# Kernel optimization log

Hardware: AMD Instinct MI355X
Metric: run time of the kernel (lower is better)

The kernel has to match this reference:

```python
import jax, jax.numpy as jnp
import numpy as np

HID = 128   # hidden_dim
NCLS = 10   # n_classes
B = 64      # number of graphs in the batched heterograph
NC, NP, NN = 100000, 400000, 150000  # component / port / net node counts
E = 400000  # edges per edge type


def setup_inputs() -> dict:
    key = jax.random.key(0)
    ks = jax.random.split(key, 32)
    f32 = jnp.float32

    def w(k, shape, fan_in):
        return jax.random.normal(k, shape, dtype=f32) * (1.0 / np.sqrt(fan_in))

    inp = {
        "h_comp": jax.random.normal(ks[0], (NC, 1), f32),
        "h_port": jax.random.normal(ks[1], (NP, 2), f32),
        "h_net": jax.random.normal(ks[2], (NN, 1), f32),
        "e_cp_src": jax.random.randint(ks[3], (E,), 0, NC, dtype=jnp.int32),
        "e_cp_dst": jax.random.randint(ks[4], (E,), 0, NP, dtype=jnp.int32),
        "e_pn_src": jax.random.randint(ks[5], (E,), 0, NP, dtype=jnp.int32),
        "e_pn_dst": jax.random.randint(ks[6], (E,), 0, NN, dtype=jnp.int32),
        "gid_comp": jnp.sort(jax.random.randint(ks[7], (NC,), 0, B, dtype=jnp.int32)),
        "gid_port": jnp.sort(jax.random.randint(ks[8], (NP,), 0, B, dtype=jnp.int32)),
        "gid_net": jnp.sort(jax.random.randint(ks[9], (NN,), 0, B, dtype=jnp.int32)),
        # GraphConv weights/biases per (layer, edge_type)
        "W1_cp": w(ks[10], (1, HID), 1), "b1_cp": jnp.zeros((HID,), f32),
        "W1_pn": w(ks[11], (2, HID), 2), "b1_pn": jnp.zeros((HID,), f32),
        "W2_cp": w(ks[12], (HID, HID), HID), "b2_cp": jnp.zeros((HID,), f32),
        "W2_pn": w(ks[13], (HID, HID), HID), "b2_pn": jnp.zeros((HID,), f32),
        "W3_cp": w(ks[14], (HID, HID), HID), "b3_cp": jnp.zeros((HID,), f32),
        "W3_pn": w(ks[15], (HID, HID), HID), "b3_pn": jnp.zeros((HID,), f32),
        # classify MLP (input dim 4 = 1+2+1 pooled original features)
        "Wc1": w(ks[16], (4, HID), 4), "bc1": jnp.zeros((HID,), f32),
        "Wc2": w(ks[17], (HID, HID), HID), "bc2": jnp.zeros((HID,), f32),
        "Wc3": w(ks[18], (HID, NCLS), HID), "bc3": jnp.zeros((NCLS,), f32),
    }
    return inp


def reference(h_comp, h_port, h_net,
              e_cp_src, e_cp_dst, e_pn_src, e_pn_dst,
              gid_comp, gid_port, gid_net,
              W1_cp, b1_cp, W1_pn, b1_pn,
              W2_cp, b2_cp, W2_pn, b2_pn,
              W3_cp, b3_cp, W3_pn, b3_pn,
              Wc1, bc1, Wc2, bc2, Wc3, bc3):
    seg = jax.ops.segment_sum

    # --- HeteroGraphConv layers (faithful to original forward, including its
    # bug: DGL HeteroGraphConv drops node types with no incoming relation, so
    # 'component' vanishes after conv1 and 'port' after conv2; conv3 runs on an
    # empty dict; conv outputs are never written back to g, hence dead code).
    # GraphConv(norm='none'): dst = sum_{edges} (x_src @ W) + b
    port1 = jax.nn.relu(seg((h_comp @ W1_cp)[e_cp_src], e_cp_dst, num_segments=NP) + b1_cp)
    net1 = jax.nn.relu(seg((h_port @ W1_pn)[e_pn_src], e_pn_dst, num_segments=NN) + b1_pn)
    net2 = jax.nn.relu(seg((port1 @ W2_pn)[e_pn_src], e_pn_dst, num_segments=NN) + b2_pn)
    # conv3: skipped entirely (no src types remain in the feature dict)
    del net1, net2  # never used by the original module's output path

    # --- dgl.mean_nodes reads g.nodes[*].data['h'] = ORIGINAL input features
    def gmean(x, gid):
        s = seg(x, gid, num_segments=B)
        c = seg(jnp.ones((x.shape[0], 1), x.dtype), gid, num_segments=B)
        return s / jnp.maximum(c, 1.0)

    hg = jnp.concatenate([gmean(h_comp, gid_comp),
                          gmean(h_port, gid_port),
                          gmean(h_net, gid_net)], axis=1)  # [B, 4]

    h = jax.nn.relu(hg @ Wc1 + bc1)
    h = jax.nn.relu(h @ Wc2 + bc2)
    return h @ Wc3 + bc3  # [B, n_classes]
```

## Files before the change

kernel.cpp:

```cpp
#include <hip/hip_runtime.h>
#include <hip/hip_bf16.h>


#define NGRAPH 64
#define NB_COMP 40
#define NB_PORT 172
#define NB_NET  44
#define GRID (NB_COMP + NB_PORT + NB_NET)


__device__ __forceinline__ float ws_read(float* p) {
    return atomicAdd(p, 0.0f);
}

template <int NF>
__device__ void reduce_type(const float* __restrict__ h, const int* __restrict__ gid, int n,
                            float* __restrict__ gsum, float* __restrict__ gcnt,
                            float (*bins)[NGRAPH][4],
                            int nblocks, int bid) {
    int nv = (n + 3) >> 2;
    int per = (nv + nblocks - 1) / nblocks;
    int start = bid * per;
    int end = min(nv, start + per);
    int set = threadIdx.x & 3;

    int cur = -1;
    float s0 = 0.f, s1 = 0.f, cnt = 0.f;

    for (int iv = start + (int)threadIdx.x; iv < end; iv += (int)blockDim.x) {
        int i = iv * 4;
        int g[4];
        float v0[4], v1[4];
        if (i + 3 < n) {
            int4 g4 = ((const int4*)gid)[iv];
            g[0] = g4.x; g[1] = g4.y; g[2] = g4.z; g[3] = g4.w;
            if (NF == 1) {
                float4 hv = ((const float4*)h)[iv];
                v0[0] = hv.x; v0[1] = hv.y; v0[2] = hv.z; v0[3] = hv.w;
            } else {
                float4 ha = ((const float4*)h)[iv * 2];
                float4 hb = ((const float4*)h)[iv * 2 + 1];
                v0[0] = ha.x; v1[0] = ha.y; v0[1] = ha.z; v1[1] = ha.w;
                v0[2] = hb.x; v1[2] = hb.y; v0[3] = hb.z; v1[3] = hb.w;
            }
        } else {
#pragma unroll
            for (int t = 0; t < 4; ++t) {
                if (i + t < n) {
                    g[t] = gid[i + t];
                    if (NF == 1) { v0[t] = h[i + t]; }
                    else { v0[t] = h[(i + t) * 2]; v1[t] = h[(i + t) * 2 + 1]; }
                } else {
                    g[t] = -2;
                    v0[t] = 0.f; v1[t] = 0.f;
                }
            }
        }
#pragma unroll
        for (int t = 0; t < 4; ++t) {
            if (g[t] == -2) continue;
            if (g[t] != cur) {
                if (cur >= 0) {
                    atomicAdd(&bins[set][cur][0], s0);
                    if (NF == 2) atomicAdd(&bins[set][cur][1], s1);
                    atomicAdd(&bins[set][cur][2], cnt);
                }
                cur = g[t]; s0 = 0.f; s1 = 0.f; cnt = 0.f;
            }
            s0 += v0[t];
            if (NF == 2) s1 += v1[t];
            cnt += 1.f;
        }
    }
    if (cur >= 0) {
        atomicAdd(&bins[set][cur][0], s0);
        if (NF == 2) atomicAdd(&bins[set][cur][1], s1);
        atomicAdd(&bins[set][cur][2], cnt);
    }
    __syncthreads();

    for (int g = threadIdx.x; g < NGRAPH; g += blockDim.x) {
        float c = bins[0][g][2] + bins[1][g][2] + bins[2][g][2] + bins[3][g][2];
        if (c != 0.f) {
            float a0 = bins[0][g][0] + bins[1][g][0] + bins[2][g][0] + bins[3][g][0];
            if (NF == 1) {
                atomicAdd(&gsum[g], a0);
            } else {
                float a1 = bins[0][g][1] + bins[1][g][1] + bins[2][g][1] + bins[3][g][1];
                atomicAdd(&gsum[g * 2 + 0], a0);
                atomicAdd(&gsum[g * 2 + 1], a1);
            }
            atomicAdd(&gcnt[g], c);
        }
    }
}

__global__ __launch_bounds__(256) void fused_kernel(
    const float* __restrict__ h_comp, const float* __restrict__ h_port,
    const float* __restrict__ h_net,
    const int* __restrict__ gid_comp, const int* __restrict__ gid_port,
    const int* __restrict__ gid_net,
    int n_comp, int n_port, int n_net,
    const float* __restrict__ Wc1, const float* __restrict__ bc1,
    const float* __restrict__ Wc2, const float* __restrict__ bc2,
    const float* __restrict__ Wc3, const float* __restrict__ bc3,
    float* __restrict__ ws, float* __restrict__ out) {
    __shared__ float bins[4][NGRAPH][4];
    __shared__ int ticket;
    __shared__ float hgs[4];
    __shared__ float h1[128];
    __shared__ float part[2][128];
    __shared__ float h2[128];
    __shared__ float l3[16][12];

    int tid = threadIdx.x;
    int bid = blockIdx.x;
    int* counter = (int*)(ws + 448);

    for (int i = tid; i < 4 * NGRAPH * 4; i += blockDim.x) ((float*)bins)[i] = 0.f;
    __syncthreads();

    if (bid < NB_COMP) {
        reduce_type<1>(h_comp, gid_comp, n_comp, ws + 0, ws + 64, bins, NB_COMP, bid);
    } else if (bid < NB_COMP + NB_PORT) {
        reduce_type<2>(h_port, gid_port, n_port, ws + 128, ws + 256, bins, NB_PORT, bid - NB_COMP);
    } else {
        reduce_type<1>(h_net, gid_net, n_net, ws + 320, ws + 384, bins, NB_NET, bid - NB_COMP - NB_PORT);
    }
    __syncthreads();

    if (tid == 0) {
        __threadfence();
        ticket = atomicAdd(counter, 1);
    }
    __syncthreads();
    int my = ticket;
    if (my >= NGRAPH) return;

    int g = my;
    if (tid == 0) {
        while (atomicAdd(counter, 0) < GRID) __builtin_amdgcn_s_sleep(2);
        float cc = fmaxf(ws_read(ws + 64 + g), 1.f);
        float cp = fmaxf(ws_read(ws + 256 + g), 1.f);
        float cn = fmaxf(ws_read(ws + 384 + g), 1.f);
        hgs[0] = ws_read(ws + g) / cc;
        hgs[1] = ws_read(ws + 128 + 2 * g) / cp;
        hgs[2] = ws_read(ws + 128 + 2 * g + 1) / cp;
        hgs[3] = ws_read(ws + 320 + g) / cn;
    }
    __syncthreads();

    if (tid < 128) {
        float v = hgs[0] * Wc1[tid] + hgs[1] * Wc1[128 + tid] +
                  hgs[2] * Wc1[256 + tid] + hgs[3] * Wc1[384 + tid] + bc1[tid];
        h1[tid] = fmaxf(v, 0.f);
    }
    __syncthreads();

    {
        int j = tid & 127;
        int h = tid >> 7;
        float acc = 0.f;
#pragma unroll
        for (int kk = 0; kk < 64; kk += 4) {
            int k = h * 64 + kk;
            float4 hh = *(const float4*)&h1[k];
            acc += hh.x * Wc2[(k + 0) * 128 + j] + hh.y * Wc2[(k + 1) * 128 + j] +
                   hh.z * Wc2[(k + 2) * 128 + j] + hh.w * Wc2[(k + 3) * 128 + j];
        }
        part[h][j] = acc;
    }
    __syncthreads();
    if (tid < 128) h2[tid] = fmaxf(part[0][tid] + part[1][tid] + bc2[tid], 0.f);
    __syncthreads();

    if (tid < 160) {
        int c = tid % 10;
        int seg = tid / 10;
        float a = 0.f;
#pragma unroll
        for (int k = seg * 8; k < seg * 8 + 8; ++k) a += h2[k] * Wc3[k * 10 + c];
        l3[seg][c] = a;
    }
    __syncthreads();
    if (tid < 10) {
        float a = bc3[tid];
#pragma unroll
        for (int s = 0; s < 16; ++s) a += l3[s][tid];
        out[g * 10 + tid] = a;
    }
}

extern "C" void kernel_launch(void* const* d_in, const int* in_sizes, int n_in,
                              void* d_out, int out_size, void* d_ws, size_t ws_size,
                              hipStream_t stream) {
    const float* h_comp = (const float*)d_in[0];
    const float* h_port = (const float*)d_in[1];
    const float* h_net  = (const float*)d_in[2];
    const int* gid_comp = (const int*)d_in[7];
    const int* gid_port = (const int*)d_in[8];
    const int* gid_net  = (const int*)d_in[9];
    const float* Wc1 = (const float*)d_in[22];
    const float* bc1 = (const float*)d_in[23];
    const float* Wc2 = (const float*)d_in[24];
    const float* bc2 = (const float*)d_in[25];
    const float* Wc3 = (const float*)d_in[26];
    const float* bc3 = (const float*)d_in[27];

    int n_comp = in_sizes[0];
    int n_port = in_sizes[1] / 2;
    int n_net  = in_sizes[2];

    float* ws = (float*)d_ws;
    float* out = (float*)d_out;

    hipMemsetAsync(ws, 0, 452 * sizeof(float), stream);

    fused_kernel<<<GRID, 256, 0, stream>>>(
        h_comp, h_port, h_net, gid_comp, gid_port, gid_net,
        n_comp, n_port, n_net,
        Wc1, bc1, Wc2, bc2, Wc3, bc3, ws, out);
}
```

Measured before the change: 129.1 us.

## Split fused kernel into reduce and MLP kernels with per-block partials

The single fused kernel used global atomics plus a ticket counter and spin-wait before the MLP. It becomes two launches: a reduce kernel with about four times as many blocks, each writing its per-graph partial sums to a dedicated slot with no atomics, and an MLP kernel with one block per graph that sums the slots. This drops the memset, the global atomics and the spin-wait, at the cost of an extra launch and a larger workspace read.

```diff
diff --git a/kernel.cpp b/kernel.cpp
--- a/kernel.cpp
+++ b/kernel.cpp
@@ -3,19 +3,14 @@
 
 
 #define NGRAPH 64
-#define NB_COMP 40
-#define NB_PORT 172
-#define NB_NET  44
-#define GRID (NB_COMP + NB_PORT + NB_NET)
-
-
-__device__ __forceinline__ float ws_read(float* p) {
-    return atomicAdd(p, 0.0f);
-}
+#define NB_COMP 120
+#define NB_PORT 723
+#define NB_NET  181
+#define NSLOT (NB_COMP + NB_PORT + NB_NET)
+
 
 template <int NF>
 __device__ void reduce_type(const float* __restrict__ h, const int* __restrict__ gid, int n,
-                            float* __restrict__ gsum, float* __restrict__ gcnt,
                             float (*bins)[NGRAPH][4],
                             int nblocks, int bid) {
     int nv = (n + 3) >> 2;
@@ -77,76 +72,87 @@
         if (NF == 2) atomicAdd(&bins[set][cur][1], s1);
         atomicAdd(&bins[set][cur][2], cnt);
     }
-    __syncthreads();
-
-    for (int g = threadIdx.x; g < NGRAPH; g += blockDim.x) {
-        float c = bins[0][g][2] + bins[1][g][2] + bins[2][g][2] + bins[3][g][2];
-        if (c != 0.f) {
-            float a0 = bins[0][g][0] + bins[1][g][0] + bins[2][g][0] + bins[3][g][0];
-            if (NF == 1) {
-                atomicAdd(&gsum[g], a0);
-            } else {
-                float a1 = bins[0][g][1] + bins[1][g][1] + bins[2][g][1] + bins[3][g][1];
-                atomicAdd(&gsum[g * 2 + 0], a0);
-                atomicAdd(&gsum[g * 2 + 1], a1);
-            }
-            atomicAdd(&gcnt[g], c);
-        }
-    }
-}
-
-__global__ __launch_bounds__(256) void fused_kernel(
+}
+
+__global__ __launch_bounds__(256) void reduce_kernel(
     const float* __restrict__ h_comp, const float* __restrict__ h_port,
     const float* __restrict__ h_net,
     const int* __restrict__ gid_comp, const int* __restrict__ gid_port,
     const int* __restrict__ gid_net,
     int n_comp, int n_port, int n_net,
+    float4* __restrict__ ws4) {
+    __shared__ float bins[4][NGRAPH][4];
+    int tid = threadIdx.x;
+    int bid = blockIdx.x;
+
+    for (int i = tid; i < 4 * NGRAPH * 4; i += blockDim.x) ((float*)bins)[i] = 0.f;
+    __syncthreads();
+
+    if (bid < NB_COMP) {
+        reduce_type<1>(h_comp, gid_comp, n_comp, bins, NB_COMP, bid);
+    } else if (bid < NB_COMP + NB_PORT) {
+        reduce_type<2>(h_port, gid_port, n_port, bins, NB_PORT, bid - NB_COMP);
+    } else {
+        reduce_type<1>(h_net, gid_net, n_net, bins, NB_NET, bid - NB_COMP - NB_PORT);
+    }
+    __syncthreads();
+
+    if (tid < NGRAPH) {
+        float s0 = bins[0][tid][0] + bins[1][tid][0] + bins[2][tid][0] + bins[3][tid][0];
+        float s1 = bins[0][tid][1] + bins[1][tid][1] + bins[2][tid][1] + bins[3][tid][1];
+        float c  = bins[0][tid][2] + bins[1][tid][2] + bins[2][tid][2] + bins[3][tid][2];
+        ws4[(size_t)tid * NSLOT + bid] = make_float4(s0, s1, c, 0.f);
+    }
+}
+
+__global__ __launch_bounds__(256) void mlp_kernel(
+    const float4* __restrict__ ws4,
     const float* __restrict__ Wc1, const float* __restrict__ bc1,
     const float* __restrict__ Wc2, const float* __restrict__ bc2,
     const float* __restrict__ Wc3, const float* __restrict__ bc3,
-    float* __restrict__ ws, float* __restrict__ out) {
-    __shared__ float bins[4][NGRAPH][4];
-    __shared__ int ticket;
+    float* __restrict__ out) {
+    __shared__ float wred[4][8];
     __shared__ float hgs[4];
     __shared__ float h1[128];
     __shared__ float part[2][128];
     __shared__ float h2[128];
     __shared__ float l3[16][12];
 
+    int g = blockIdx.x;
     int tid = threadIdx.x;
-    int bid = blockIdx.x;
-    int* counter = (int*)(ws + 448);
-
-    for (int i = tid; i < 4 * NGRAPH * 4; i += blockDim.x) ((float*)bins)[i] = 0.f;
-    __syncthreads();
-
-    if (bid < NB_COMP) {
-        reduce_type<1>(h_comp, gid_comp, n_comp, ws + 0, ws + 64, bins, NB_COMP, bid);
-    } else if (bid < NB_COMP + NB_PORT) {
-        reduce_type<2>(h_port, gid_port, n_port, ws + 128, ws + 256, bins, NB_PORT, bid - NB_COMP);
-    } else {
-        reduce_type<1>(h_net, gid_net, n_net, ws + 320, ws + 384, bins, NB_NET, bid - NB_COMP - NB_PORT);
-    }
-    __syncthreads();
-
+
+    float cs = 0.f, cc = 0.f, p0 = 0.f, p1 = 0.f, pc = 0.f, ns = 0.f, nc = 0.f;
+    for (int s = tid; s < NSLOT; s += 256) {
+        float4 v = ws4[(size_t)g * NSLOT + s];
+        if (s < NB_COMP) { cs += v.x; cc += v.z; }
+        else if (s < NB_COMP + NB_PORT) { p0 += v.x; p1 += v.y; pc += v.z; }
+        else { ns += v.x; nc += v.z; }
+    }
+#pragma unroll
+    for (int off = 32; off > 0; off >>= 1) {
+        cs += __shfl_down(cs, off); cc += __shfl_down(cc, off);
+        p0 += __shfl_down(p0, off); p1 += __shfl_down(p1, off);
+        pc += __shfl_down(pc, off); ns += __shfl_down(ns, off);
+        nc += __shfl_down(nc, off);
+    }
+    int wave = tid >> 6;
+    if ((tid & 63) == 0) {
+        wred[wave][0] = cs; wred[wave][1] = cc; wred[wave][2] = p0; wred[wave][3] = p1;
+        wred[wave][4] = pc; wred[wave][5] = ns; wred[wave][6] = nc;
+    }
+    __syncthreads();
     if (tid == 0) {
-        __threadfence();
-        ticket = atomicAdd(counter, 1);
-    }
-    __syncthreads();
-    int my = ticket;
-    if (my >= NGRAPH) return;
-
-    int g = my;
-    if (tid == 0) {
-        while (atomicAdd(counter, 0) < GRID) __builtin_amdgcn_s_sleep(2);
-        float cc = fmaxf(ws_read(ws + 64 + g), 1.f);
-        float cp = fmaxf(ws_read(ws + 256 + g), 1.f);
-        float cn = fmaxf(ws_read(ws + 384 + g), 1.f);
-        hgs[0] = ws_read(ws + g) / cc;
-        hgs[1] = ws_read(ws + 128 + 2 * g) / cp;
-        hgs[2] = ws_read(ws + 128 + 2 * g + 1) / cp;
-        hgs[3] = ws_read(ws + 320 + g) / cn;
+        float t0 = wred[0][0] + wred[1][0] + wred[2][0] + wred[3][0];
+        float t1 = wred[0][1] + wred[1][1] + wred[2][1] + wred[3][1];
+        float t2 = wred[0][2] + wred[1][2] + wred[2][2] + wred[3][2];
+        float t3 = wred[0][3] + wred[1][3] + wred[2][3] + wred[3][3];
+        float t4 = wred[0][4] + wred[1][4] + wred[2][4] + wred[3][4];
+        float t5 = wred[0][5] + wred[1][5] + wred[2][5] + wred[3][5];
+        float t6 = wred[0][6] + wred[1][6] + wred[2][6] + wred[3][6];
+        hgs[0] = t0 / fmaxf(t1, 1.f);
+        hgs[1] = t2 / fmaxf(t4, 1.f);
+        hgs[2] = t3 / fmaxf(t4, 1.f);
+        hgs[3] = t5 / fmaxf(t6, 1.f);
     }
     __syncthreads();
 
@@ -211,13 +217,12 @@
     int n_port = in_sizes[1] / 2;
     int n_net  = in_sizes[2];
 
-    float* ws = (float*)d_ws;
+    float4* ws4 = (float4*)d_ws;
     float* out = (float*)d_out;
 
-    hipMemsetAsync(ws, 0, 452 * sizeof(float), stream);
-
-    fused_kernel<<<GRID, 256, 0, stream>>>(
+    reduce_kernel<<<NSLOT, 256, 0, stream>>>(
         h_comp, h_port, h_net, gid_comp, gid_port, gid_net,
-        n_comp, n_port, n_net,
-        Wc1, bc1, Wc2, bc2, Wc3, bc3, ws, out);
-}
+        n_comp, n_port, n_net, ws4);
+
+    mlp_kernel<<<NGRAPH, 256, 0, stream>>>(ws4, Wc1, bc1, Wc2, bc2, Wc3, bc3, out);
+}
```

Result: faster. 117.7 us (-8.8%).
